# Performance work log

Measured on AMD Instinct MI355X. Metric: run time of the kernel, lower is better.

Reference implementation:

```python
import jax, jax.numpy as jnp
import numpy as np

B, D_IN, H0, H1, LAT, C = 8192, 2048, 1024, 512, 128, 8
SCALE = 0.02  # weight init scale to keep activations well-conditioned


def _unshared_linear_relu(x, labels, W, b):
    """Per-cluster Linear+ReLU routing. x:[B,din], W:[C,din,dout], b:[C,dout].
    Computes all cluster branches then selects per-row branch (same math as
    torch's mask gather->Linear->scatter; rows never reorder)."""
    y = jax.nn.relu(jnp.einsum('bi,cio->bco', x, W) + b[None, :, :])  # [B,C,dout]
    return jnp.take_along_axis(y, labels[:, None, None], axis=1)[:, 0, :]


def setup_inputs() -> dict:
    key = jax.random.key(0)
    ks = jax.random.split(key, 12)
    return {
        'x': jax.random.normal(ks[0], (B, D_IN), dtype=jnp.float32),
        'cluster_labels': jax.random.randint(ks[1], (B,), 0, C, dtype=jnp.int32),
        'eps': jax.random.normal(ks[2], (B, LAT), dtype=jnp.float32),
        'W_enc0': jax.random.normal(ks[3], (C, D_IN, H0), dtype=jnp.float32) * SCALE,
        'b_enc0': jnp.zeros((C, H0), dtype=jnp.float32),
        'W_enc1': jax.random.normal(ks[4], (H0, H1), dtype=jnp.float32) * SCALE,
        'b_enc1': jnp.zeros((H1,), dtype=jnp.float32),
        'W_mu': jax.random.normal(ks[5], (H1, LAT), dtype=jnp.float32) * SCALE,
        'b_mu': jnp.zeros((LAT,), dtype=jnp.float32),
        'W_logvar': jax.random.normal(ks[6], (H1, LAT), dtype=jnp.float32) * SCALE,
        'b_logvar': jnp.zeros((LAT,), dtype=jnp.float32),
        'W_dec0': jax.random.normal(ks[7], (LAT, H1), dtype=jnp.float32) * SCALE,
        'b_dec0': jnp.zeros((H1,), dtype=jnp.float32),
        'W_dec1': jax.random.normal(ks[8], (C, H1, H0), dtype=jnp.float32) * SCALE,
        'b_dec1': jnp.zeros((C, H0), dtype=jnp.float32),
        'W_out': jax.random.normal(ks[9], (H0, D_IN), dtype=jnp.float32) * SCALE,
        'b_out': jnp.zeros((D_IN,), dtype=jnp.float32),
    }


def reference(x, cluster_labels, eps,
              W_enc0, b_enc0, W_enc1, b_enc1,
              W_mu, b_mu, W_logvar, b_logvar,
              W_dec0, b_dec0, W_dec1, b_dec1,
              W_out, b_out):
    labels = cluster_labels.astype(jnp.int32)
    # encoder: unshared layer 0, shared layer 1
    h = _unshared_linear_relu(x, labels, W_enc0, b_enc0)          # [B, H0]
    h = jax.nn.relu(h @ W_enc1 + b_enc1)                          # [B, H1]
    # shared latent heads
    mu = h @ W_mu + b_mu                                          # [B, LAT]
    logvar = h @ W_logvar + b_logvar                              # [B, LAT]
    # reparameterize
    z = mu + eps * jnp.exp(0.5 * logvar)                          # [B, LAT]
    # decoder: shared layer 0, unshared layer 1 (hidden_dims reversed)
    d = jax.nn.relu(z @ W_dec0 + b_dec0)                          # [B, H1]
    d = _unshared_linear_relu(d, labels, W_dec1, b_dec1)          # [B, H0]
    # shared output layer (no activation)
    recon = d @ W_out + b_out                                     # [B, D_IN]
    return recon, mu, logvar
```

## Files before the change

### kernel.cpp

```cpp
#include <hip/hip_runtime.h>


#define DEVI __device__ __forceinline__

constexpr int B_    = 8192;
constexpr int DIN   = 2048;
constexpr int H0_   = 1024;
constexpr int H1_   = 512;
constexpr int LAT_  = 128;
constexpr int NC    = 8;

constexpr int BM = 128, BN = 128, BK = 32;
constexpr int TCAP   = 72;
constexpr int BP_CAP = TCAP * BM;

#define MI_CURSOR 0
#define MI_NTILES 8
#define MI_TILEC  16

typedef __attribute__((ext_vector_type(8))) short bf16x8;
typedef __attribute__((ext_vector_type(4))) float f32x4;
typedef const __attribute__((address_space(1))) unsigned int* gas_uint_ptr;
typedef __attribute__((address_space(3))) unsigned int* las_uint_ptr;

DEVI unsigned short f2bf(float f) {
  union { float f; unsigned u; } a; a.f = f;
  unsigned r = a.u + 0x7fffu + ((a.u >> 16) & 1u);
  return (unsigned short)(r >> 16);
}

DEVI void gll16(const unsigned short* g, unsigned short* l) {
  __builtin_amdgcn_global_load_lds((gas_uint_ptr)g, (las_uint_ptr)l, 16, 0, 0);
}

constexpr size_t AL256(size_t x) { return (x + 255) & ~(size_t)255; }
constexpr size_t OFF_META = 0;
constexpr size_t OFF_PERM = 512;
constexpr size_t OFF_XG   = AL256(OFF_PERM + (size_t)BP_CAP * 4);
constexpr size_t OFF_H0   = AL256(OFF_XG  + (size_t)BP_CAP * DIN * 2);
constexpr size_t OFF_H1   = AL256(OFF_H0  + (size_t)BP_CAP * H0_ * 2);
constexpr size_t OFF_MLP  = AL256(OFF_H1  + (size_t)BP_CAP * H1_ * 2);
constexpr size_t OFF_BML  = AL256(OFF_MLP + (size_t)BP_CAP * 256 * 4);
constexpr size_t OFF_WT0  = AL256(OFF_BML + 256 * 4);
constexpr size_t OFF_WT1  = AL256(OFF_WT0 + (size_t)NC * DIN * H0_ * 2);
constexpr size_t OFF_WML  = AL256(OFF_WT1 + (size_t)H0_ * H1_ * 2);
constexpr size_t OFF_WD0  = AL256(OFF_WML + (size_t)256 * H1_ * 2);
constexpr size_t OFF_WD1  = AL256(OFF_WD0 + (size_t)LAT_ * H1_ * 2);
constexpr size_t OFF_WOUT = AL256(OFF_WD1 + (size_t)NC * H1_ * H0_ * 2);

__global__ void setup_a(const int* __restrict__ labels, int* __restrict__ meta,
                        int* __restrict__ perm) {
  __shared__ int cnt[NC];
  int t = threadIdx.x;
  if (t < NC) cnt[t] = 0;
  __syncthreads();
  for (int i = t; i < B_; i += 256) atomicAdd(&cnt[labels[i]], 1);
  for (int i = t; i < BP_CAP; i += 256) perm[i] = -1;
  __syncthreads();
  if (t == 0) {
    int off = 0, nt = 0;
    for (int c = 0; c < NC; ++c) {
      meta[MI_CURSOR + c] = off;
      int k = (cnt[c] + BM - 1) >> 7;
      for (int j = 0; j < k; ++j) meta[MI_TILEC + nt + j] = c;
      nt += k;
      off += k << 7;
    }
    meta[MI_NTILES] = nt;
  }
}

__global__ void setup_b(const int* __restrict__ labels, int* __restrict__ meta,
                        int* __restrict__ perm) {
  int i = blockIdx.x * 256 + threadIdx.x;
  if (i < B_) {
    int pos = atomicAdd(&meta[MI_CURSOR + labels[i]], 1);
    perm[pos] = i;
  }
}

__global__ void concat_bias(const float* __restrict__ a, const float* __restrict__ b,
                            float* __restrict__ o) {
  int j = threadIdx.x;
  o[j] = (j < 128) ? a[j] : b[j - 128];
}

__global__ void convert_transpose(const float* __restrict__ src, unsigned short* __restrict__ dst,
                                  int K, int N) {
  __shared__ float t[32][33];
  const float* s = src + (size_t)blockIdx.z * K * N;
  unsigned short* d = dst + (size_t)blockIdx.z * K * N;
  int n0 = blockIdx.x * 32, k0 = blockIdx.y * 32;
  for (int i = threadIdx.y; i < 32; i += 8)
    t[i][threadIdx.x] = s[(size_t)(k0 + i) * N + n0 + threadIdx.x];
  __syncthreads();
  for (int i = threadIdx.y; i < 32; i += 8)
    d[(size_t)(n0 + i) * K + k0 + threadIdx.x] = f2bf(t[threadIdx.x][i]);
}

__global__ void gather_x_kernel(const float* __restrict__ x, const int* __restrict__ perm,
                                unsigned short* __restrict__ xg) {
  int p = blockIdx.x;
  int c4 = blockIdx.y * 256 + threadIdx.x;
  int src = perm[p];
  float4 v = make_float4(0.f, 0.f, 0.f, 0.f);
  if (src >= 0) v = ((const float4*)(x + (size_t)src * DIN))[c4];
  ushort4 o;
  o.x = f2bf(v.x); o.y = f2bf(v.y); o.z = f2bf(v.z); o.w = f2bf(v.w);
  ((ushort4*)(xg + (size_t)p * DIN))[c4] = o;
}

__global__ void z_kernel(const float* __restrict__ mlp, const float* __restrict__ eps,
                         const int* __restrict__ perm, unsigned short* __restrict__ z,
                         float* __restrict__ out_mu, float* __restrict__ out_lv) {
  int p = blockIdx.x, j = threadIdx.x;
  int src = perm[p];
  float zz = 0.f;
  if (src >= 0) {
    float m = mlp[(size_t)p * 256 + j];
    float l = mlp[(size_t)p * 256 + 128 + j];
    zz = m + eps[(size_t)src * LAT_ + j] * expf(0.5f * l);
    out_mu[(size_t)src * LAT_ + j] = m;
    out_lv[(size_t)src * LAT_ + j] = l;
  }
  z[(size_t)p * LAT_ + j] = f2bf(zz);
}

template <int OUT_MODE, bool RELU, bool PCW, bool PCB>
__global__ __launch_bounds__(256, 2)
void gemm_kernel(const unsigned short* __restrict__ A,
                 const unsigned short* __restrict__ Bt,
                 const float* __restrict__ bias,
                 void* __restrict__ Cout,
                 const int* __restrict__ meta,
                 const int* __restrict__ perm,
                 int K, int N, int ldc) {
  const int ntiles = meta[MI_NTILES];
  const int tm = blockIdx.x;
  if (tm >= ntiles) return;
  const int tn = blockIdx.y;

  int cluster = 0;
  if (PCW || PCB) cluster = meta[MI_TILEC + tm];
  const unsigned short* Bp = Bt + (PCW ? (size_t)cluster * (size_t)N * K : 0);
  const float* bb = bias + (PCB ? (size_t)cluster * N : 0);

  __shared__ alignas(16) unsigned short As[BM][BK];
  __shared__ alignas(16) unsigned short Bs[BN][BK];

  const int tid  = threadIdx.x;
  const int w    = tid >> 6, lane = tid & 63;
  const int fr   = lane & 15, quad = lane >> 4;
  const int wm   = (w >> 1) * 64, wn = (w & 1) * 64;

  const int c0 = (w * 2 + 0) * 64 + lane;
  const int c1 = (w * 2 + 1) * 64 + lane;
  const size_t aoff0 = (size_t)(tm * BM + (c0 >> 2)) * K + (c0 & 3) * 8;
  const size_t aoff1 = (size_t)(tm * BM + (c1 >> 2)) * K + (c1 & 3) * 8;
  const size_t boff0 = (size_t)(tn * BN + (c0 >> 2)) * K + (c0 & 3) * 8;
  const size_t boff1 = (size_t)(tn * BN + (c1 >> 2)) * K + (c1 & 3) * 8;
  unsigned short* lA0 = &As[0][0] + (w * 2 + 0) * 512;
  unsigned short* lA1 = &As[0][0] + (w * 2 + 1) * 512;
  unsigned short* lB0 = &Bs[0][0] + (w * 2 + 0) * 512;
  unsigned short* lB1 = &Bs[0][0] + (w * 2 + 1) * 512;

  f32x4 acc[4][4] = {};

  for (int k0 = 0; k0 < K; k0 += BK) {
    gll16(A  + aoff0 + k0, lA0);
    gll16(A  + aoff1 + k0, lA1);
    gll16(Bp + boff0 + k0, lB0);
    gll16(Bp + boff1 + k0, lB1);
    __syncthreads();

    bf16x8 af[4], bf[4];
#pragma unroll
    for (int i = 0; i < 4; ++i) af[i] = *(const bf16x8*)&As[wm + i * 16 + fr][quad * 8];
#pragma unroll
    for (int i = 0; i < 4; ++i) bf[i] = *(const bf16x8*)&Bs[wn + i * 16 + fr][quad * 8];
#pragma unroll
    for (int mi = 0; mi < 4; ++mi)
#pragma unroll
      for (int ni = 0; ni < 4; ++ni)
        acc[mi][ni] = __builtin_amdgcn_mfma_f32_16x16x32_bf16(af[mi], bf[ni], acc[mi][ni], 0, 0, 0);
    __syncthreads();
  }

  float bv[4];
#pragma unroll
  for (int ni = 0; ni < 4; ++ni) bv[ni] = bb[tn * BN + wn + ni * 16 + fr];

#pragma unroll
  for (int mi = 0; mi < 4; ++mi) {
#pragma unroll
    for (int r = 0; r < 4; ++r) {
      int m = tm * BM + wm + mi * 16 + quad * 4 + r;
      int orow = m;
      if (OUT_MODE == 2) orow = perm[m];
#pragma unroll
      for (int ni = 0; ni < 4; ++ni) {
        int n = tn * BN + wn + ni * 16 + fr;
        float v = acc[mi][ni][r] + bv[ni];
        if (RELU) v = fmaxf(v, 0.f);
        if (OUT_MODE == 0) {
          ((unsigned short*)Cout)[(size_t)m * N + n] = f2bf(v);
        } else if (OUT_MODE == 1) {
          ((float*)Cout)[(size_t)m * N + n] = v;
        } else {
          if (orow >= 0) ((float*)Cout)[(size_t)orow * ldc + n] = v;
        }
      }
    }
  }
}

extern "C" void kernel_launch(void* const* d_in, const int* in_sizes, int n_in,
                              void* d_out, int out_size, void* d_ws, size_t ws_size,
                              hipStream_t stream) {
  const float* x        = (const float*)d_in[0];
  const int*   labels   = (const int*)d_in[1];
  const float* eps      = (const float*)d_in[2];
  const float* W_enc0   = (const float*)d_in[3];
  const float* b_enc0   = (const float*)d_in[4];
  const float* W_enc1   = (const float*)d_in[5];
  const float* b_enc1   = (const float*)d_in[6];
  const float* W_mu     = (const float*)d_in[7];
  const float* b_mu     = (const float*)d_in[8];
  const float* W_logvar = (const float*)d_in[9];
  const float* b_logvar = (const float*)d_in[10];
  const float* W_dec0   = (const float*)d_in[11];
  const float* b_dec0   = (const float*)d_in[12];
  const float* W_dec1   = (const float*)d_in[13];
  const float* b_dec1   = (const float*)d_in[14];
  const float* W_out    = (const float*)d_in[15];
  const float* b_out    = (const float*)d_in[16];

  float* out_recon = (float*)d_out;
  float* out_mu    = out_recon + (size_t)B_ * DIN;
  float* out_lv    = out_mu + (size_t)B_ * LAT_;

  char* ws = (char*)d_ws;
  int* meta            = (int*)(ws + OFF_META);
  int* perm            = (int*)(ws + OFF_PERM);
  unsigned short* xg   = (unsigned short*)(ws + OFF_XG);
  unsigned short* h0   = (unsigned short*)(ws + OFF_H0);
  unsigned short* h1   = (unsigned short*)(ws + OFF_H1);
  float* mlp           = (float*)(ws + OFF_MLP);
  float* b_ml          = (float*)(ws + OFF_BML);
  unsigned short* Wt0  = (unsigned short*)(ws + OFF_WT0);
  unsigned short* Wt1  = (unsigned short*)(ws + OFF_WT1);
  unsigned short* Wml  = (unsigned short*)(ws + OFF_WML);
  unsigned short* Wd0  = (unsigned short*)(ws + OFF_WD0);
  unsigned short* Wd1  = (unsigned short*)(ws + OFF_WD1);
  unsigned short* Wout = (unsigned short*)(ws + OFF_WOUT);
  unsigned short* d1 = xg;
  unsigned short* d0 = h0;
  unsigned short* z  = h1;

  dim3 cb(32, 8);

  setup_a<<<1, 256, 0, stream>>>(labels, meta, perm);
  setup_b<<<(B_ + 255) / 256, 256, 0, stream>>>(labels, meta, perm);
  concat_bias<<<1, 256, 0, stream>>>(b_mu, b_logvar, b_ml);

  convert_transpose<<<dim3(H0_ / 32, DIN / 32, NC), cb, 0, stream>>>(W_enc0, Wt0, DIN, H0_);
  convert_transpose<<<dim3(H1_ / 32, H0_ / 32, 1), cb, 0, stream>>>(W_enc1, Wt1, H0_, H1_);
  convert_transpose<<<dim3(LAT_ / 32, H1_ / 32, 1), cb, 0, stream>>>(W_mu, Wml, H1_, LAT_);
  convert_transpose<<<dim3(LAT_ / 32, H1_ / 32, 1), cb, 0, stream>>>(W_logvar, Wml + (size_t)LAT_ * H1_, H1_, LAT_);
  convert_transpose<<<dim3(H1_ / 32, LAT_ / 32, 1), cb, 0, stream>>>(W_dec0, Wd0, LAT_, H1_);
  convert_transpose<<<dim3(H0_ / 32, H1_ / 32, NC), cb, 0, stream>>>(W_dec1, Wd1, H1_, H0_);
  convert_transpose<<<dim3(DIN / 32, H0_ / 32, 1), cb, 0, stream>>>(W_out, Wout, H0_, DIN);

  gather_x_kernel<<<dim3(BP_CAP, DIN / (256 * 4)), 256, 0, stream>>>(x, perm, xg);

  gemm_kernel<0, true, true, true><<<dim3(TCAP, H0_ / BN), 256, 0, stream>>>(
      xg, Wt0, b_enc0, h0, meta, perm, DIN, H0_, 0);
  gemm_kernel<0, true, false, false><<<dim3(TCAP, H1_ / BN), 256, 0, stream>>>(
      h0, Wt1, b_enc1, h1, meta, perm, H0_, H1_, 0);
  gemm_kernel<1, false, false, false><<<dim3(TCAP, 256 / BN), 256, 0, stream>>>(
      h1, Wml, b_ml, mlp, meta, perm, H1_, 256, 0);
  z_kernel<<<BP_CAP, 128, 0, stream>>>(mlp, eps, perm, z, out_mu, out_lv);
  gemm_kernel<0, true, false, false><<<dim3(TCAP, H1_ / BN), 256, 0, stream>>>(
      z, Wd0, b_dec0, d0, meta, perm, LAT_, H1_, 0);
  gemm_kernel<0, true, true, true><<<dim3(TCAP, H0_ / BN), 256, 0, stream>>>(
      d0, Wd1, b_dec1, d1, meta, perm, H1_, H0_, 0);
  gemm_kernel<2, false, false, false><<<dim3(TCAP, DIN / BN), 256, 0, stream>>>(
      d1, Wout, b_out, out_recon, meta, perm, H0_, DIN, DIN);

  (void)in_sizes; (void)n_in; (void)out_size; (void)ws_size;
}
```

Before: 508.6 us.

## Double-buffer GEMM LDS with XOR swizzle and merge setup/convert launches

```diff
diff --git a/kernel.cpp b/kernel.cpp
--- a/kernel.cpp
+++ b/kernel.cpp
@@ -14,7 +14,6 @@
 constexpr int TCAP   = 72;
 constexpr int BP_CAP = TCAP * BM;
 
-#define MI_CURSOR 0
 #define MI_NTILES 8
 #define MI_TILEC  16
 
@@ -48,19 +47,21 @@
 constexpr size_t OFF_WD1  = AL256(OFF_WD0 + (size_t)LAT_ * H1_ * 2);
 constexpr size_t OFF_WOUT = AL256(OFF_WD1 + (size_t)NC * H1_ * H0_ * 2);
 
-__global__ void setup_a(const int* __restrict__ labels, int* __restrict__ meta,
-                        int* __restrict__ perm) {
-  __shared__ int cnt[NC];
+__global__ void setup_all(const int* __restrict__ labels, int* __restrict__ meta,
+                          int* __restrict__ perm, const float* __restrict__ b_mu,
+                          const float* __restrict__ b_lv, float* __restrict__ b_ml) {
+  __shared__ int cnt[NC], base[NC];
   int t = threadIdx.x;
   if (t < NC) cnt[t] = 0;
-  __syncthreads();
-  for (int i = t; i < B_; i += 256) atomicAdd(&cnt[labels[i]], 1);
-  for (int i = t; i < BP_CAP; i += 256) perm[i] = -1;
+  if (t < 256) b_ml[t] = (t < 128) ? b_mu[t] : b_lv[t - 128];
+  __syncthreads();
+  for (int i = t; i < B_; i += 1024) atomicAdd(&cnt[labels[i]], 1);
+  for (int i = t; i < BP_CAP; i += 1024) perm[i] = -1;
   __syncthreads();
   if (t == 0) {
     int off = 0, nt = 0;
     for (int c = 0; c < NC; ++c) {
-      meta[MI_CURSOR + c] = off;
+      base[c] = off;
       int k = (cnt[c] + BM - 1) >> 7;
       for (int j = 0; j < k; ++j) meta[MI_TILEC + nt + j] = c;
       nt += k;
@@ -68,34 +69,37 @@
     }
     meta[MI_NTILES] = nt;
   }
-}
-
-__global__ void setup_b(const int* __restrict__ labels, int* __restrict__ meta,
-                        int* __restrict__ perm) {
-  int i = blockIdx.x * 256 + threadIdx.x;
-  if (i < B_) {
-    int pos = atomicAdd(&meta[MI_CURSOR + labels[i]], 1);
+  __syncthreads();
+  if (t < NC) cnt[t] = base[t];
+  __syncthreads();
+  for (int i = t; i < B_; i += 1024) {
+    int pos = atomicAdd(&cnt[labels[i]], 1);
     perm[pos] = i;
   }
 }
 
-__global__ void concat_bias(const float* __restrict__ a, const float* __restrict__ b,
-                            float* __restrict__ o) {
-  int j = threadIdx.x;
-  o[j] = (j < 128) ? a[j] : b[j - 128];
-}
-
-__global__ void convert_transpose(const float* __restrict__ src, unsigned short* __restrict__ dst,
-                                  int K, int N) {
-  __shared__ float t[32][33];
-  const float* s = src + (size_t)blockIdx.z * K * N;
-  unsigned short* d = dst + (size_t)blockIdx.z * K * N;
-  int n0 = blockIdx.x * 32, k0 = blockIdx.y * 32;
+struct SegDesc { const float* src; unsigned short* dst; int K, N, nb, tstart; };
+struct SegTable { SegDesc s[7]; };
+
+__global__ void convert_all(SegTable t) {
+  __shared__ float tl[32][33];
+  int tile = blockIdx.x;
+  int si = 0;
+#pragma unroll
+  for (int i = 1; i < 7; ++i) si += (tile >= t.s[i].tstart) ? 1 : 0;
+  const SegDesc sd = t.s[si];
+  int local = tile - sd.tstart;
+  int tpb = (sd.K >> 5) * (sd.N >> 5);
+  int b = local / tpb, rem = local - b * tpb;
+  int tk = rem / (sd.N >> 5), tn = rem - tk * (sd.N >> 5);
+  const float* s = sd.src + (size_t)b * sd.K * sd.N;
+  unsigned short* d = sd.dst + (size_t)b * sd.K * sd.N;
+  int n0 = tn * 32, k0 = tk * 32;
   for (int i = threadIdx.y; i < 32; i += 8)
-    t[i][threadIdx.x] = s[(size_t)(k0 + i) * N + n0 + threadIdx.x];
+    tl[i][threadIdx.x] = s[(size_t)(k0 + i) * sd.N + n0 + threadIdx.x];
   __syncthreads();
   for (int i = threadIdx.y; i < 32; i += 8)
-    d[(size_t)(n0 + i) * K + k0 + threadIdx.x] = f2bf(t[threadIdx.x][i]);
+    d[(size_t)(n0 + i) * sd.K + k0 + threadIdx.x] = f2bf(tl[threadIdx.x][i]);
 }
 
 __global__ void gather_x_kernel(const float* __restrict__ x, const int* __restrict__ perm,
@@ -135,9 +139,8 @@
                  const int* __restrict__ meta,
                  const int* __restrict__ perm,
                  int K, int N, int ldc) {
-  const int ntiles = meta[MI_NTILES];
   const int tm = blockIdx.x;
-  if (tm >= ntiles) return;
+  if (tm >= meta[MI_NTILES]) return;
   const int tn = blockIdx.y;
 
   int cluster = 0;
@@ -145,45 +148,74 @@
   const unsigned short* Bp = Bt + (PCW ? (size_t)cluster * (size_t)N * K : 0);
   const float* bb = bias + (PCB ? (size_t)cluster * N : 0);
 
-  __shared__ alignas(16) unsigned short As[BM][BK];
-  __shared__ alignas(16) unsigned short Bs[BN][BK];
+  __shared__ alignas(16) unsigned short As[2][BM * BK];
+  __shared__ alignas(16) unsigned short Bs[2][BN * BK];
 
   const int tid  = threadIdx.x;
   const int w    = tid >> 6, lane = tid & 63;
   const int fr   = lane & 15, quad = lane >> 4;
   const int wm   = (w >> 1) * 64, wn = (w & 1) * 64;
 
-  const int c0 = (w * 2 + 0) * 64 + lane;
-  const int c1 = (w * 2 + 1) * 64 + lane;
-  const size_t aoff0 = (size_t)(tm * BM + (c0 >> 2)) * K + (c0 & 3) * 8;
-  const size_t aoff1 = (size_t)(tm * BM + (c1 >> 2)) * K + (c1 & 3) * 8;
-  const size_t boff0 = (size_t)(tn * BN + (c0 >> 2)) * K + (c0 & 3) * 8;
-  const size_t boff1 = (size_t)(tn * BN + (c1 >> 2)) * K + (c1 & 3) * 8;
-  unsigned short* lA0 = &As[0][0] + (w * 2 + 0) * 512;
-  unsigned short* lA1 = &As[0][0] + (w * 2 + 1) * 512;
-  unsigned short* lB0 = &Bs[0][0] + (w * 2 + 0) * 512;
-  unsigned short* lB1 = &Bs[0][0] + (w * 2 + 1) * 512;
+  const int s0 = (w * 2 + 0) * 64 + lane;
+  const int s1 = (w * 2 + 1) * 64 + lane;
+  const int r0 = s0 >> 2, r1 = s1 >> 2;
+  const int c0 = (s0 & 3) ^ ((r0 >> 1) & 3);
+  const int c1 = (s1 & 3) ^ ((r1 >> 1) & 3);
+  const size_t aoff0 = (size_t)(tm * BM + r0) * K + c0 * 8;
+  const size_t aoff1 = (size_t)(tm * BM + r1) * K + c1 * 8;
+  const size_t boff0 = (size_t)(tn * BN + r0) * K + c0 * 8;
+  const size_t boff1 = (size_t)(tn * BN + r1) * K + c1 * 8;
+  const int l0 = s0 * 8, l1 = s1 * 8;
+
+  int aro[4], bro[4];
+#pragma unroll
+  for (int i = 0; i < 4; ++i) {
+    int R = wm + i * 16 + fr;
+    aro[i] = (R * 4 + (quad ^ ((R >> 1) & 3))) * 8;
+    R = wn + i * 16 + fr;
+    bro[i] = (R * 4 + (quad ^ ((R >> 1) & 3))) * 8;
+  }
 
   f32x4 acc[4][4] = {};
 
-  for (int k0 = 0; k0 < K; k0 += BK) {
-    gll16(A  + aoff0 + k0, lA0);
-    gll16(A  + aoff1 + k0, lA1);
-    gll16(Bp + boff0 + k0, lB0);
-    gll16(Bp + boff1 + k0, lB1);
+  gll16(A  + aoff0, &As[0][l0]);
+  gll16(A  + aoff1, &As[0][l1]);
+  gll16(Bp + boff0, &Bs[0][l0]);
+  gll16(Bp + boff1, &Bs[0][l1]);
+
+  int cur = 0;
+  for (int k0 = BK; k0 < K; k0 += BK) {
     __syncthreads();
-
-    bf16x8 af[4], bf[4];
-#pragma unroll
-    for (int i = 0; i < 4; ++i) af[i] = *(const bf16x8*)&As[wm + i * 16 + fr][quad * 8];
-#pragma unroll
-    for (int i = 0; i < 4; ++i) bf[i] = *(const bf16x8*)&Bs[wn + i * 16 + fr][quad * 8];
+    const int nxt = cur ^ 1;
+    gll16(A  + aoff0 + k0, &As[nxt][l0]);
+    gll16(A  + aoff1 + k0, &As[nxt][l1]);
+    gll16(Bp + boff0 + k0, &Bs[nxt][l0]);
+    gll16(Bp + boff1 + k0, &Bs[nxt][l1]);
+
+    bf16x8 af[4], bfr[4];
+#pragma unroll
+    for (int i = 0; i < 4; ++i) af[i]  = *(const bf16x8*)&As[cur][aro[i]];
+#pragma unroll
+    for (int i = 0; i < 4; ++i) bfr[i] = *(const bf16x8*)&Bs[cur][bro[i]];
 #pragma unroll
     for (int mi = 0; mi < 4; ++mi)
 #pragma unroll
       for (int ni = 0; ni < 4; ++ni)
-        acc[mi][ni] = __builtin_amdgcn_mfma_f32_16x16x32_bf16(af[mi], bf[ni], acc[mi][ni], 0, 0, 0);
-    __syncthreads();
+        acc[mi][ni] = __builtin_amdgcn_mfma_f32_16x16x32_bf16(af[mi], bfr[ni], acc[mi][ni], 0, 0, 0);
+    cur = nxt;
+  }
+  __syncthreads();
+  {
+    bf16x8 af[4], bfr[4];
+#pragma unroll
+    for (int i = 0; i < 4; ++i) af[i]  = *(const bf16x8*)&As[cur][aro[i]];
+#pragma unroll
+    for (int i = 0; i < 4; ++i) bfr[i] = *(const bf16x8*)&Bs[cur][bro[i]];
+#pragma unroll
+    for (int mi = 0; mi < 4; ++mi)
+#pragma unroll
+      for (int ni = 0; ni < 4; ++ni)
+        acc[mi][ni] = __builtin_amdgcn_mfma_f32_16x16x32_bf16(af[mi], bfr[ni], acc[mi][ni], 0, 0, 0);
   }
 
   float bv[4];
@@ -257,20 +289,22 @@
   unsigned short* d0 = h0;
   unsigned short* z  = h1;
 
-  dim3 cb(32, 8);
-
-  setup_a<<<1, 256, 0, stream>>>(labels, meta, perm);
-  setup_b<<<(B_ + 255) / 256, 256, 0, stream>>>(labels, meta, perm);
-  concat_bias<<<1, 256, 0, stream>>>(b_mu, b_logvar, b_ml);
-
-  convert_transpose<<<dim3(H0_ / 32, DIN / 32, NC), cb, 0, stream>>>(W_enc0, Wt0, DIN, H0_);
-  convert_transpose<<<dim3(H1_ / 32, H0_ / 32, 1), cb, 0, stream>>>(W_enc1, Wt1, H0_, H1_);
-  convert_transpose<<<dim3(LAT_ / 32, H1_ / 32, 1), cb, 0, stream>>>(W_mu, Wml, H1_, LAT_);
-  convert_transpose<<<dim3(LAT_ / 32, H1_ / 32, 1), cb, 0, stream>>>(W_logvar, Wml + (size_t)LAT_ * H1_, H1_, LAT_);
-  convert_transpose<<<dim3(H1_ / 32, LAT_ / 32, 1), cb, 0, stream>>>(W_dec0, Wd0, LAT_, H1_);
-  convert_transpose<<<dim3(H0_ / 32, H1_ / 32, NC), cb, 0, stream>>>(W_dec1, Wd1, H1_, H0_);
-  convert_transpose<<<dim3(DIN / 32, H0_ / 32, 1), cb, 0, stream>>>(W_out, Wout, H0_, DIN);
-
+  SegTable st;
+  int ts = 0;
+  auto seg = [&](int i, const float* s, unsigned short* d, int K, int N, int nb) {
+    st.s[i] = SegDesc{s, d, K, N, nb, ts};
+    ts += (K / 32) * (N / 32) * nb;
+  };
+  seg(0, W_enc0,   Wt0,                      DIN,  H0_,  NC);
+  seg(1, W_enc1,   Wt1,                      H0_,  H1_,  1);
+  seg(2, W_mu,     Wml,                      H1_,  LAT_, 1);
+  seg(3, W_logvar, Wml + (size_t)LAT_ * H1_, H1_,  LAT_, 1);
+  seg(4, W_dec0,   Wd0,                      LAT_, H1_,  1);
+  seg(5, W_dec1,   Wd1,                      H1_,  H0_,  NC);
+  seg(6, W_out,    Wout,                     H0_,  DIN,  1);
+
+  setup_all<<<1, 1024, 0, stream>>>(labels, meta, perm, b_mu, b_logvar, b_ml);
+  convert_all<<<ts, dim3(32, 8), 0, stream>>>(st);
   gather_x_kernel<<<dim3(BP_CAP, DIN / (256 * 4)), 256, 0, stream>>>(x, perm, xg);
 
   gemm_kernel<0, true, true, true><<<dim3(TCAP, H0_ / BN), 256, 0, stream>>>(
```

Result: faster. 445.1 us (-12.5%).
